# Kernel optimization log

Hardware: AMD Instinct MI355X
Metric: run time of the kernel (lower is better)

The kernel has to match this reference:

```python
import jax, jax.numpy as jnp
import numpy as np

KQ_DIM = 132  # latent_dim == kq_dim so gather covers full rows
EPS = 1e-12


def setup_inputs() -> dict:
    key = jax.random.key(0)
    ks = jax.random.split(key, 8)
    B, C, H, W = 8, 3, 128, 128
    N, K, D = 2048, 32, KQ_DIM
    indices = jax.random.randint(ks[0], (3, B, N, K), 0, H * W + 1, dtype=jnp.int32)
    img = jax.random.normal(ks[1], (B, C, H, W), dtype=jnp.float32)
    # stand-in backbone: 3x3 conv (ResidualDenseNetwork not in source)
    conv_w = jax.random.normal(ks[2], (D, C, 3, 3), dtype=jnp.float32) * (1.0 / np.sqrt(C * 9))
    conv_b = jnp.zeros((D,), dtype=jnp.float32)
    sc = 1.0 / np.sqrt(D)
    ks_w = jax.random.normal(ks[3], (D, D), dtype=jnp.float32) * sc
    ks_b = jax.random.normal(ks[4], (D,), dtype=jnp.float32) * sc
    qs_w = jax.random.normal(ks[5], (D, D), dtype=jnp.float32) * sc
    qs_b = jax.random.normal(ks[6], (D,), dtype=jnp.float32) * sc
    return {"indices": indices, "img": img, "conv_w": conv_w, "conv_b": conv_b,
            "ks_w": ks_w, "ks_b": ks_b, "qs_w": qs_w, "qs_b": qs_b}


def reference(indices, img, conv_w, conv_b, ks_w, ks_b, qs_w, qs_b):
    _, B, N, K = indices.shape
    # backbone conv: [B, D, H, W]
    feat = jax.lax.conv_general_dilated(
        img, conv_w, window_strides=(1, 1), padding='SAME',
        dimension_numbers=('NCHW', 'OIHW', 'NCHW')) + conv_b[None, :, None, None]
    # torch F.normalize(dim=-1) BEFORE permute -> L2 over last spatial (width) axis
    norm = jnp.linalg.norm(feat, axis=-1, keepdims=True)
    feat = feat / jnp.maximum(norm, EPS)
    # permute(0,2,3,1): [B, H, W, D] -> flatten spatial
    feat = jnp.transpose(feat, (0, 2, 3, 1))
    Bf, Hh, Ww, D = feat.shape
    flat = feat.reshape(Bf, Hh * Ww, D)
    flat = jnp.concatenate([flat, jnp.zeros((Bf, 1, D), dtype=flat.dtype)], axis=1)
    flat_ks = flat @ ks_w.T + ks_b  # [B, WH+1, D]
    flat_qs = flat @ qs_w.T + qs_b
    x_idx = indices[1].reshape(B, N * K)  # [B, N*K]
    y_idx = indices[2].reshape(B, N * K)
    x_feat = jnp.take_along_axis(flat_ks, x_idx[:, :, None], axis=1).reshape(B, N, K, D)
    y_feat = jnp.take_along_axis(flat_qs, y_idx[:, :, None], axis=1).reshape(B, N, K, D)
    # entailment logits: scaled dot product over feature dim
    logits = (x_feat * y_feat).sum(axis=-1) * (D ** -0.5)  # [B, N, K]
    return logits
```

## Files before the change

### kernel.cpp

```cpp
#include <hip/hip_runtime.h>
#include <hip/hip_bf16.h>
#include <math.h>

#define B_ 8
#define H_ 128
#define W_ 128
#define C_ 3
#define D_ 132
#define HW_ (H_*W_)
#define RPB_ (HW_+1)
#define NROWS_ (B_*RPB_)
#define AROWS_ 131136
#define FSTRIDE_ 136
#define MSTRIDE_ 168
#define MROWS_ 136
#define MELEMS_ (MROWS_*MSTRIDE_)
#define MALLOC_ 24192
#define NK_ 65536
#define NOUT_ (B_*NK_)

typedef __attribute__((ext_vector_type(8))) short short8v;
typedef __attribute__((ext_vector_type(8))) unsigned short ushort8v;
typedef __attribute__((ext_vector_type(4))) float f32x4;

__device__ inline float bf2f(unsigned short u) {
  return __uint_as_float(((unsigned)u) << 16);
}
__device__ inline unsigned short f2bf(float f) {
  __hip_bfloat16 hb = __float2bfloat16(f);
  return *(unsigned short*)&hb;
}

__global__ __launch_bounds__(512) void prep_kernel(
    const float* __restrict__ ks_w, const float* __restrict__ ks_b,
    const float* __restrict__ qs_w, const float* __restrict__ qs_b,
    unsigned short* __restrict__ Mb, float* __restrict__ cc) {
  int idx = blockIdx.x * 512 + threadIdx.x;
  if (idx >= MALLOC_) return;
  float val = 0.f;
  if (idx < MELEMS_) {
    int a = idx / MSTRIDE_;
    int k = idx - a * MSTRIDE_;
    if (k < D_) {
      if (a < D_) {
        for (int o = 0; o < D_; ++o)
          val = fmaf(ks_w[o * D_ + a], qs_w[o * D_ + k], val);
      } else if (a == 132) {
        for (int o = 0; o < D_; ++o)
          val = fmaf(qs_b[o], ks_w[o * D_ + k], val);
      } else if (a == 133) {
        for (int o = 0; o < D_; ++o)
          val = fmaf(ks_b[o], qs_w[o * D_ + k], val);
      }
    }
  }
  Mb[idx] = f2bf(val);
  if (idx == 0) {
    float s = 0.f;
    for (int o = 0; o < D_; ++o) s = fmaf(ks_b[o], qs_b[o], s);
    cc[0] = s;
  }
}

__device__ __forceinline__ float conv_item16(
    const float* __restrict__ in_s, const float* __restrict__ w_s,
    float bias, int d, int w0, float* acc) {
  float wt[27];
#pragma unroll
  for (int j = 0; j < 27; ++j) wt[j] = w_s[d * 27 + j];
#pragma unroll
  for (int i = 0; i < 16; ++i) acc[i] = bias;
#pragma unroll
  for (int ck = 0; ck < 9; ++ck) {
    const float4* p4 = (const float4*)(in_s + ck * 132);
    float v[20];
#pragma unroll
    for (int j = 0; j < 5; ++j) {
      float4 t4 = p4[(w0 >> 2) + j];
      v[4 * j + 0] = t4.x; v[4 * j + 1] = t4.y;
      v[4 * j + 2] = t4.z; v[4 * j + 3] = t4.w;
    }
#pragma unroll
    for (int i = 0; i < 16; ++i) {
      float a0 = fmaf(v[i], wt[ck * 3 + 0], acc[i]);
      float a1 = fmaf(v[i + 1], wt[ck * 3 + 1], a0);
      acc[i] = fmaf(v[i + 2], wt[ck * 3 + 2], a1);
    }
  }
  float ssq = 0.f;
#pragma unroll
  for (int i = 0; i < 16; ++i) ssq = fmaf(acc[i], acc[i], ssq);
  return ssq;
}

__global__ __launch_bounds__(512, 4) void fused_conv_gemm_kernel(
    const float* __restrict__ img, const float* __restrict__ cw,
    const float* __restrict__ cb, unsigned short* __restrict__ fmain,
    unsigned short* __restrict__ ft, const unsigned short* __restrict__ Mb,
    const float* __restrict__ cc, unsigned short* __restrict__ zmain,
    unsigned short* __restrict__ zt) {
  int bid = blockIdx.x;
  int tid = threadIdx.x;

  if (bid == B_ * H_) {
    float cval = cc[0];
    for (int i = tid; i < B_ * 128; i += 512) {
      int b = i >> 7, c = i & 127;
      size_t r = (size_t)b * RPB_ + HW_;
      fmain[r * 128 + c] = 0;
      zmain[r * 128 + c] = 0;
    }
    if (tid < B_) {
      size_t r = (size_t)tid * RPB_ + HW_;
      ushort8v f8 = {0, 0, 0, 0, 0x3F80, 0, 0, 0};
      *(ushort8v*)(ft + r * 8) = f8;
      ushort8v z8 = {0, 0, 0, 0, f2bf(cval), 0x3F80, 0, 0};
      *(ushort8v*)(zt + r * 8) = z8;
    }
    return;
  }

  int wave = tid >> 6, lane = tid & 63;
  __shared__ __align__(16) float nscale[132];
  __shared__ __align__(16) char un[34880];
  float* in_s = (float*)un;
  float* w_s  = in_s + 9 * 132;
  float* b_s  = w_s + 132 * 27;
  float* parts = b_s + 132;
  unsigned short* As = (unsigned short*)un;
  unsigned short* su_s = (unsigned short*)nscale;

  int b = bid >> 7, h = bid & 127;
  for (int i = tid; i < 9 * 132; i += 512) {
    int ck = i / 132, x = i - ck * 132;
    int c = ck / 3, kh = ck - c * 3;
    int hh = h + kh - 1, ww = x - 1;
    float val = 0.f;
    if (x >= 1 && x <= 128 && hh >= 0 && hh < H_)
      val = img[((size_t)(b * C_ + c) * H_ + hh) * W_ + ww];
    in_s[i] = val;
  }
  for (int i = tid; i < D_ * 27; i += 512) w_s[i] = cw[i];
  if (tid < D_) b_s[tid] = cb[tid];
  __syncthreads();

  float acc0[16], acc1[16], acc2[16];
  int i0 = tid, i1 = tid + 512;
  int wg0 = i0 / 132, dd0 = i0 - wg0 * 132;
  int wg1 = i1 / 132, dd1 = i1 - wg1 * 132;
  parts[wg0 * 132 + dd0] = conv_item16(in_s, w_s, b_s[dd0], dd0, wg0 * 16, acc0);
  parts[wg1 * 132 + dd1] = conv_item16(in_s, w_s, b_s[dd1], dd1, wg1 * 16, acc1);
  int dd2 = 0;
  if (tid < 32) {
    dd2 = 100 + tid;
    parts[7 * 132 + dd2] = conv_item16(in_s, w_s, b_s[dd2], dd2, 112, acc2);
  }
  __syncthreads();
  if (tid < 132) {
    float s = 0.f;
#pragma unroll
    for (int rr = 0; rr < 8; ++rr) s += parts[rr * 132 + tid];
    nscale[tid] = 1.f / fmaxf(sqrtf(s), 1e-12f);
  }
  __syncthreads();

  {
    float sc = nscale[dd0];
#pragma unroll
    for (int i = 0; i < 16; ++i)
      As[(wg0 * 16 + i) * FSTRIDE_ + dd0] = f2bf(acc0[i] * sc);
    sc = nscale[dd1];
#pragma unroll
    for (int i = 0; i < 16; ++i)
      As[(wg1 * 16 + i) * FSTRIDE_ + dd1] = f2bf(acc1[i] * sc);
  }
  if (tid < 32) {
    float sc = nscale[dd2];
#pragma unroll
    for (int i = 0; i < 16; ++i)
      As[(112 + i) * FSTRIDE_ + dd2] = f2bf(acc2[i] * sc);
  }
  if (tid < 128) {
    uint2 tv; tv.x = 0x3F80u; tv.y = 0u;
    *(uint2*)&As[tid * FSTRIDE_ + 132] = tv;
  }
  if (tid < 32) As[128 * FSTRIDE_ + tid] = 0;
  __syncthreads();

  size_t rowbase = (size_t)b * RPB_ + (size_t)h * W_;
  unsigned short* fmb = fmain + rowbase * 128;
  for (int i2 = tid; i2 < 2048; i2 += 512) {
    int r = i2 >> 4, c8 = i2 & 15;
    *(ushort8v*)(fmb + r * 128 + c8 * 8) = *(const ushort8v*)(As + r * FSTRIDE_ + c8 * 8);
  }
  uint2 ftl = {0, 0};
  if (tid < 128) ftl = *(const uint2*)&As[tid * FSTRIDE_ + 128];

  int c15 = lane & 15, kg = lane >> 4;
  const unsigned short* arow = As + (wave * 16 + c15) * FSTRIDE_ + kg * 8;
  const unsigned short* browg = Mb + c15 * MSTRIDE_ + kg * 8;
  f32x4 acc[9] = {};
#pragma unroll
  for (int ks = 0; ks < 5; ++ks) {
    short8v af = *(const short8v*)(arow + ks * 32);
#pragma unroll
    for (int ct = 0; ct < 9; ++ct) {
      short8v bf = *(const short8v*)(browg + ct * 16 * MSTRIDE_ + ks * 32);
      acc[ct] = __builtin_amdgcn_mfma_f32_16x16x32_bf16(af, bf, acc[ct], 0, 0, 0);
    }
  }
  __syncthreads();

  float cval = cc[0];
  int r0 = wave * 16 + kg * 4;
#pragma unroll
  for (int ct = 0; ct < 9; ++ct) {
    int col = ct * 16 + c15;
#pragma unroll
    for (int j = 0; j < 4; ++j) {
      int r = r0 + j;
      if (col < D_)            As[r * FSTRIDE_ + col] = f2bf(acc[ct][j]);
      else if (col == 132)     su_s[r] = f2bf(acc[ct][j]);
      else if (col == 133)     As[r * FSTRIDE_ + 132] = f2bf(acc[ct][j] + cval);
      else if (col == 134)     As[r * FSTRIDE_ + 133] = 0x3F80;
      else if (col == 135)     As[r * FSTRIDE_ + 134] = 0;
      else if (col == 136)     As[r * FSTRIDE_ + 135] = 0;
    }
  }
  __syncthreads();

  unsigned short* zmb = zmain + rowbase * 128;
  for (int i2 = tid; i2 < 2048; i2 += 512) {
    int r = i2 >> 4, c8 = i2 & 15;
    *(ushort8v*)(zmb + r * 128 + c8 * 8) = *(const ushort8v*)(As + r * FSTRIDE_ + c8 * 8);
  }
  if (tid < 128) {
    *(ushort8v*)(zt + (rowbase + tid) * 8) = *(const ushort8v*)(As + tid * FSTRIDE_ + 128);
    ushort8v f8;
    f8[0] = (unsigned short)(ftl.x & 0xFFFFu);
    f8[1] = (unsigned short)(ftl.x >> 16);
    f8[2] = (unsigned short)(ftl.y & 0xFFFFu);
    f8[3] = (unsigned short)(ftl.y >> 16);
    f8[4] = 0x3F80;
    f8[5] = su_s[tid];
    f8[6] = 0;
    f8[7] = 0;
    *(ushort8v*)(ft + (rowbase + tid) * 8) = f8;
  }
}

__global__ __launch_bounds__(256) void gather_kernel(
    const int* __restrict__ xi, const int* __restrict__ yi,
    const unsigned short* __restrict__ fmain, const unsigned short* __restrict__ ft,
    const unsigned short* __restrict__ zmain, const unsigned short* __restrict__ zt,
    float* __restrict__ out) {
  const float scale = 0.08703882797784892f;
  int bi = blockIdx.x;
  int b = bi & 7;
  int chunk = bi >> 3;
  int lane = threadIdx.x & 7;
  int rem1 = chunk * 32 + (threadIdx.x >> 3);
  int rem2 = rem1 + 32768;

  size_t ib1 = (size_t)b * NK_ + rem1;
  size_t ib2 = (size_t)b * NK_ + rem2;
  int x1 = xi[ib1], y1 = yi[ib1];
  int x2 = xi[ib2], y2 = yi[ib2];
  size_t bbase = (size_t)b * RPB_;
  const unsigned short* fx1 = fmain + (bbase + x1) * 128;
  const unsigned short* zy1 = zmain + (bbase + y1) * 128;
  const unsigned short* fx2 = fmain + (bbase + x2) * 128;
  const unsigned short* zy2 = zmain + (bbase + y2) * 128;

  int e0 = lane * 16;
  ushort8v a10 = *(const ushort8v*)(fx1 + e0);
  ushort8v a11 = *(const ushort8v*)(fx1 + e0 + 8);
  ushort8v z10 = *(const ushort8v*)(zy1 + e0);
  ushort8v z11 = *(const ushort8v*)(zy1 + e0 + 8);
  ushort8v a20 = *(const ushort8v*)(fx2 + e0);
  ushort8v a21 = *(const ushort8v*)(fx2 + e0 + 8);
  ushort8v z20 = *(const ushort8v*)(zy2 + e0);
  ushort8v z21 = *(const ushort8v*)(zy2 + e0 + 8);
  unsigned short a1t = ft[(bbase + x1) * 8 + lane];
  unsigned short z1t = zt[(bbase + y1) * 8 + lane];
  unsigned short a2t = ft[(bbase + x2) * 8 + lane];
  unsigned short z2t = zt[(bbase + y2) * 8 + lane];

  float acc1 = bf2f(a1t) * bf2f(z1t);
  float acc2 = bf2f(a2t) * bf2f(z2t);
#pragma unroll
  for (int t = 0; t < 8; ++t) {
    acc1 = fmaf(bf2f(a10[t]), bf2f(z10[t]), acc1);
    acc2 = fmaf(bf2f(a20[t]), bf2f(z20[t]), acc2);
  }
#pragma unroll
  for (int t = 0; t < 8; ++t) {
    acc1 = fmaf(bf2f(a11[t]), bf2f(z11[t]), acc1);
    acc2 = fmaf(bf2f(a21[t]), bf2f(z21[t]), acc2);
  }
  acc1 += __shfl_xor(acc1, 1);
  acc2 += __shfl_xor(acc2, 1);
  acc1 += __shfl_xor(acc1, 2);
  acc2 += __shfl_xor(acc2, 2);
  acc1 += __shfl_xor(acc1, 4);
  acc2 += __shfl_xor(acc2, 4);
  if (lane == 0) {
    out[((size_t)b << 16) | rem1] = acc1 * scale;
    out[((size_t)b << 16) | rem2] = acc2 * scale;
  }
}

extern "C" void kernel_launch(void* const* d_in, const int* in_sizes, int n_in,
                              void* d_out, int out_size, void* d_ws, size_t ws_size,
                              hipStream_t stream) {
  const int* indices  = (const int*)d_in[0];
  const float* img    = (const float*)d_in[1];
  const float* conv_w = (const float*)d_in[2];
  const float* conv_b = (const float*)d_in[3];
  const float* ks_w   = (const float*)d_in[4];
  const float* ks_b   = (const float*)d_in[5];
  const float* qs_w   = (const float*)d_in[6];
  const float* qs_b   = (const float*)d_in[7];
  float* out = (float*)d_out;

  char* w = (char*)d_ws;
  unsigned short* fmain = (unsigned short*)w;
  size_t off = (size_t)AROWS_ * 128 * 2;
  unsigned short* zmain = (unsigned short*)(w + off); off += (size_t)AROWS_ * 128 * 2;
  unsigned short* ftl = (unsigned short*)(w + off);   off += (size_t)AROWS_ * 8 * 2;
  unsigned short* ztl = (unsigned short*)(w + off);   off += (size_t)AROWS_ * 8 * 2;
  unsigned short* Mb = (unsigned short*)(w + off);    off += MALLOC_ * 2;
  float* cc = (float*)(w + off);

  const int* xi = indices + (size_t)B_ * NK_;
  const int* yi = indices + (size_t)2 * B_ * NK_;

  hipLaunchKernelGGL(prep_kernel, dim3((MALLOC_ + 511) / 512), dim3(512), 0, stream,
                     ks_w, ks_b, qs_w, qs_b, Mb, cc);
  hipLaunchKernelGGL(fused_conv_gemm_kernel, dim3(B_ * H_ + 1), dim3(512), 0, stream,
                     img, conv_w, conv_b, fmain, ftl, Mb, cc, zmain, ztl);
  hipLaunchKernelGGL(gather_kernel, dim3(NOUT_ / 64), dim3(256), 0, stream,
                     xi, yi, fmain, ftl, zmain, ztl, out);
}
```

Measured before the change: 89.25 us.

## Compute 3x3 conv via split-bf16 MFMA im2col instead of scalar FMAs

Replaces the per-thread scalar FMA convolution with an im2col GEMM on matrix cores. Weights and bias are pre-split in the prep kernel into bf16 high and low parts. Patches are built in LDS as hi/lo bf16, and three MFMAs per tile recover near-fp32 accuracy. Row norms are reduced with lane shuffles. This aims to cut the ALU-bound conv cost, at the price of a small precision loss and extra prep work.

```diff
diff --git a/kernel.cpp b/kernel.cpp
--- a/kernel.cpp
+++ b/kernel.cpp
@@ -16,6 +16,7 @@
 #define MROWS_ 136
 #define MELEMS_ (MROWS_*MSTRIDE_)
 #define MALLOC_ 24192
+#define WELEMS_ 4608
 #define NK_ 65536
 #define NOUT_ (B_*NK_)
 
@@ -34,69 +35,54 @@
 __global__ __launch_bounds__(512) void prep_kernel(
     const float* __restrict__ ks_w, const float* __restrict__ ks_b,
     const float* __restrict__ qs_w, const float* __restrict__ qs_b,
-    unsigned short* __restrict__ Mb, float* __restrict__ cc) {
+    const float* __restrict__ cw, const float* __restrict__ cb,
+    unsigned short* __restrict__ Mb, unsigned short* __restrict__ Whb,
+    unsigned short* __restrict__ Wlb, float* __restrict__ cc) {
   int idx = blockIdx.x * 512 + threadIdx.x;
-  if (idx >= MALLOC_) return;
-  float val = 0.f;
-  if (idx < MELEMS_) {
-    int a = idx / MSTRIDE_;
-    int k = idx - a * MSTRIDE_;
-    if (k < D_) {
-      if (a < D_) {
-        for (int o = 0; o < D_; ++o)
-          val = fmaf(ks_w[o * D_ + a], qs_w[o * D_ + k], val);
-      } else if (a == 132) {
-        for (int o = 0; o < D_; ++o)
-          val = fmaf(qs_b[o], ks_w[o * D_ + k], val);
-      } else if (a == 133) {
-        for (int o = 0; o < D_; ++o)
-          val = fmaf(ks_b[o], qs_w[o * D_ + k], val);
+  if (idx < MALLOC_) {
+    float val = 0.f;
+    if (idx < MELEMS_) {
+      int a = idx / MSTRIDE_;
+      int k = idx - a * MSTRIDE_;
+      if (k < D_) {
+        if (a < D_) {
+          for (int o = 0; o < D_; ++o)
+            val = fmaf(ks_w[o * D_ + a], qs_w[o * D_ + k], val);
+        } else if (a == 132) {
+          for (int o = 0; o < D_; ++o)
+            val = fmaf(qs_b[o], ks_w[o * D_ + k], val);
+        } else if (a == 133) {
+          for (int o = 0; o < D_; ++o)
+            val = fmaf(ks_b[o], qs_w[o * D_ + k], val);
+        }
       }
     }
-  }
-  Mb[idx] = f2bf(val);
-  if (idx == 0) {
-    float s = 0.f;
-    for (int o = 0; o < D_; ++o) s = fmaf(ks_b[o], qs_b[o], s);
-    cc[0] = s;
-  }
-}
-
-__device__ __forceinline__ float conv_item16(
-    const float* __restrict__ in_s, const float* __restrict__ w_s,
-    float bias, int d, int w0, float* acc) {
-  float wt[27];
-#pragma unroll
-  for (int j = 0; j < 27; ++j) wt[j] = w_s[d * 27 + j];
-#pragma unroll
-  for (int i = 0; i < 16; ++i) acc[i] = bias;
-#pragma unroll
-  for (int ck = 0; ck < 9; ++ck) {
-    const float4* p4 = (const float4*)(in_s + ck * 132);
-    float v[20];
-#pragma unroll
-    for (int j = 0; j < 5; ++j) {
-      float4 t4 = p4[(w0 >> 2) + j];
-      v[4 * j + 0] = t4.x; v[4 * j + 1] = t4.y;
-      v[4 * j + 2] = t4.z; v[4 * j + 3] = t4.w;
-    }
-#pragma unroll
-    for (int i = 0; i < 16; ++i) {
-      float a0 = fmaf(v[i], wt[ck * 3 + 0], acc[i]);
-      float a1 = fmaf(v[i + 1], wt[ck * 3 + 1], a0);
-      acc[i] = fmaf(v[i + 2], wt[ck * 3 + 2], a1);
-    }
-  }
-  float ssq = 0.f;
-#pragma unroll
-  for (int i = 0; i < 16; ++i) ssq = fmaf(acc[i], acc[i], ssq);
-  return ssq;
+    Mb[idx] = f2bf(val);
+    if (idx == 0) {
+      float s = 0.f;
+      for (int o = 0; o < D_; ++o) s = fmaf(ks_b[o], qs_b[o], s);
+      cc[0] = s;
+    }
+  } else if (idx < MALLOC_ + 2 * WELEMS_) {
+    int i2 = idx - MALLOC_;
+    int half = i2 / WELEMS_;
+    int j = i2 - half * WELEMS_;
+    int a = j >> 5, k = j & 31;
+    float val = 0.f;
+    if (a < D_) {
+      if (k < 27) val = cw[a * 27 + k];
+      else if (k == 27) val = cb[a];
+    }
+    unsigned short hi = f2bf(val);
+    if (half == 0) Whb[j] = hi;
+    else Wlb[j] = f2bf(val - bf2f(hi));
+  }
 }
 
 __global__ __launch_bounds__(512, 4) void fused_conv_gemm_kernel(
-    const float* __restrict__ img, const float* __restrict__ cw,
-    const float* __restrict__ cb, unsigned short* __restrict__ fmain,
+    const float* __restrict__ img, unsigned short* __restrict__ fmain,
     unsigned short* __restrict__ ft, const unsigned short* __restrict__ Mb,
+    const unsigned short* __restrict__ Whb, const unsigned short* __restrict__ Wlb,
     const float* __restrict__ cc, unsigned short* __restrict__ zmain,
     unsigned short* __restrict__ zt) {
   int bid = blockIdx.x;
@@ -121,12 +107,13 @@
   }
 
   int wave = tid >> 6, lane = tid & 63;
-  __shared__ __align__(16) float nscale[132];
+  int c15 = lane & 15, kg = lane >> 4;
+  __shared__ __align__(16) float nscale[144];
   __shared__ __align__(16) char un[34880];
   float* in_s = (float*)un;
-  float* w_s  = in_s + 9 * 132;
-  float* b_s  = w_s + 132 * 27;
-  float* parts = b_s + 132;
+  unsigned short* pth = (unsigned short*)(un + 4752);
+  unsigned short* ptl = (unsigned short*)(un + 14992);
+  float* parts = (float*)(un + 25232);
   unsigned short* As = (unsigned short*)un;
   unsigned short* su_s = (unsigned short*)nscale;
 
@@ -140,45 +127,79 @@
       val = img[((size_t)(b * C_ + c) * H_ + hh) * W_ + ww];
     in_s[i] = val;
   }
-  for (int i = tid; i < D_ * 27; i += 512) w_s[i] = cw[i];
-  if (tid < D_) b_s[tid] = cb[tid];
-  __syncthreads();
-
-  float acc0[16], acc1[16], acc2[16];
-  int i0 = tid, i1 = tid + 512;
-  int wg0 = i0 / 132, dd0 = i0 - wg0 * 132;
-  int wg1 = i1 / 132, dd1 = i1 - wg1 * 132;
-  parts[wg0 * 132 + dd0] = conv_item16(in_s, w_s, b_s[dd0], dd0, wg0 * 16, acc0);
-  parts[wg1 * 132 + dd1] = conv_item16(in_s, w_s, b_s[dd1], dd1, wg1 * 16, acc1);
-  int dd2 = 0;
-  if (tid < 32) {
-    dd2 = 100 + tid;
-    parts[7 * 132 + dd2] = conv_item16(in_s, w_s, b_s[dd2], dd2, 112, acc2);
+  if (tid < 256) {
+    int arr = tid >> 7, w = tid & 127;
+    unsigned short* p = (arr ? ptl : pth) + w * 40 + 28;
+    uint2 z2; z2.x = 0u; z2.y = 0u;
+    *(uint2*)p = z2;
+  }
+  __syncthreads();
+
+  for (int idx = tid; idx < 128 * 28; idx += 512) {
+    int w = idx / 28, k = idx - w * 28;
+    float val;
+    if (k == 27) {
+      val = 1.0f;
+    } else {
+      int c = k / 9, r9 = k - c * 9;
+      int kh = r9 / 3, kw = r9 - kh * 3;
+      val = in_s[(c * 3 + kh) * 132 + w + kw];
+    }
+    unsigned short hi = f2bf(val);
+    pth[w * 40 + k] = hi;
+    ptl[w * 40 + k] = f2bf(val - bf2f(hi));
+  }
+  __syncthreads();
+
+  f32x4 cacc[9] = {};
+  {
+    const unsigned short* pb = pth + (wave * 16 + c15) * 40 + kg * 8;
+    const unsigned short* pbl = ptl + (wave * 16 + c15) * 40 + kg * 8;
+    short8v bh = *(const short8v*)pb;
+    short8v bl = *(const short8v*)pbl;
+#pragma unroll
+    for (int ct = 0; ct < 9; ++ct) {
+      short8v ah = *(const short8v*)(Whb + (ct * 16 + c15) * 32 + kg * 8);
+      short8v al = *(const short8v*)(Wlb + (ct * 16 + c15) * 32 + kg * 8);
+      cacc[ct] = __builtin_amdgcn_mfma_f32_16x16x32_bf16(ah, bh, cacc[ct], 0, 0, 0);
+      cacc[ct] = __builtin_amdgcn_mfma_f32_16x16x32_bf16(al, bh, cacc[ct], 0, 0, 0);
+      cacc[ct] = __builtin_amdgcn_mfma_f32_16x16x32_bf16(ah, bl, cacc[ct], 0, 0, 0);
+    }
+  }
+
+#pragma unroll
+  for (int ct = 0; ct < 9; ++ct) {
+#pragma unroll
+    for (int j = 0; j < 4; ++j) {
+      float v = cacc[ct][j];
+      float s = v * v;
+      s += __shfl_xor(s, 1);
+      s += __shfl_xor(s, 2);
+      s += __shfl_xor(s, 4);
+      s += __shfl_xor(s, 8);
+      if (c15 == 0) parts[wave * 144 + ct * 16 + kg * 4 + j] = s;
+    }
   }
   __syncthreads();
   if (tid < 132) {
     float s = 0.f;
 #pragma unroll
-    for (int rr = 0; rr < 8; ++rr) s += parts[rr * 132 + tid];
+    for (int rr = 0; rr < 8; ++rr) s += parts[rr * 144 + tid];
     nscale[tid] = 1.f / fmaxf(sqrtf(s), 1e-12f);
   }
   __syncthreads();
 
   {
-    float sc = nscale[dd0];
-#pragma unroll
-    for (int i = 0; i < 16; ++i)
-      As[(wg0 * 16 + i) * FSTRIDE_ + dd0] = f2bf(acc0[i] * sc);
-    sc = nscale[dd1];
-#pragma unroll
-    for (int i = 0; i < 16; ++i)
-      As[(wg1 * 16 + i) * FSTRIDE_ + dd1] = f2bf(acc1[i] * sc);
-  }
-  if (tid < 32) {
-    float sc = nscale[dd2];
-#pragma unroll
-    for (int i = 0; i < 16; ++i)
-      As[(112 + i) * FSTRIDE_ + dd2] = f2bf(acc2[i] * sc);
+    int w = wave * 16 + c15;
+#pragma unroll
+    for (int ct = 0; ct < 9; ++ct) {
+#pragma unroll
+      for (int j = 0; j < 4; ++j) {
+        int d = ct * 16 + kg * 4 + j;
+        if (d < D_)
+          As[w * FSTRIDE_ + d] = f2bf(cacc[ct][j] * nscale[d]);
+      }
+    }
   }
   if (tid < 128) {
     uint2 tv; tv.x = 0x3F80u; tv.y = 0u;
@@ -196,7 +217,6 @@
   uint2 ftl = {0, 0};
   if (tid < 128) ftl = *(const uint2*)&As[tid * FSTRIDE_ + 128];
 
-  int c15 = lane & 15, kg = lane >> 4;
   const unsigned short* arow = As + (wave * 16 + c15) * FSTRIDE_ + kg * 8;
   const unsigned short* browg = Mb + c15 * MSTRIDE_ + kg * 8;
   f32x4 acc[9] = {};
@@ -330,15 +350,18 @@
   unsigned short* ftl = (unsigned short*)(w + off);   off += (size_t)AROWS_ * 8 * 2;
   unsigned short* ztl = (unsigned short*)(w + off);   off += (size_t)AROWS_ * 8 * 2;
   unsigned short* Mb = (unsigned short*)(w + off);    off += MALLOC_ * 2;
+  unsigned short* Whb = (unsigned short*)(w + off);   off += WELEMS_ * 2;
+  unsigned short* Wlb = (unsigned short*)(w + off);   off += WELEMS_ * 2;
   float* cc = (float*)(w + off);
 
   const int* xi = indices + (size_t)B_ * NK_;
   const int* yi = indices + (size_t)2 * B_ * NK_;
 
-  hipLaunchKernelGGL(prep_kernel, dim3((MALLOC_ + 511) / 512), dim3(512), 0, stream,
-                     ks_w, ks_b, qs_w, qs_b, Mb, cc);
+  int prep_total = MALLOC_ + 2 * WELEMS_;
+  hipLaunchKernelGGL(prep_kernel, dim3((prep_total + 511) / 512), dim3(512), 0, stream,
+                     ks_w, ks_b, qs_w, qs_b, conv_w, conv_b, Mb, Whb, Wlb, cc);
   hipLaunchKernelGGL(fused_conv_gemm_kernel, dim3(B_ * H_ + 1), dim3(512), 0, stream,
-                     img, conv_w, conv_b, fmain, ftl, Mb, cc, zmain, ztl);
+                     img, fmain, ftl, Mb, Whb, Wlb, cc, zmain, ztl);
   hipLaunchKernelGGL(gather_kernel, dim3(NOUT_ / 64), dim3(256), 0, stream,
                      xi, yi, fmain, ftl, zmain, ztl, out);
 }
```

New measurement: 98.86 us. +10.8%, slower.
